# Optimization experiments

Measured on AMD Instinct MI355X. Metric: run time of the kernel, lower is better.

## Reference

```python
import jax, jax.numpy as jnp
import numpy as np
import math

N, M = 512, 31
INP, EMB, ATT = 64, 64, 64
NUM_RELS = 200
SELF_LOOP_IDX = NUM_RELS  # index num_rels is the self-loop relation


def setup_inputs() -> dict:
    key = jax.random.key(0)
    ks = jax.random.split(key, 11)
    s_w = 1.0 / math.sqrt(EMB)
    return {
        "h": jax.random.normal(ks[0], (N, INP), jnp.float32),
        "msg": jax.random.normal(ks[1], (N, M, EMB), jnp.float32),
        "msg_type": jax.random.randint(ks[2], (N, M), 0, NUM_RELS, jnp.int32),
        "r_label_node": jax.random.randint(ks[3], (N,), 0, NUM_RELS, jnp.int32),
        "r_label_msg": jax.random.randint(ks[4], (N, M), 0, NUM_RELS, jnp.int32),
        "W_self": jax.random.normal(ks[5], (INP, EMB), jnp.float32) * s_w,
        "Q": jax.random.normal(ks[6], (NUM_RELS + 1, EMB, ATT), jnp.float32) * s_w,
        "K": jax.random.normal(ks[7], (NUM_RELS + 1, EMB, ATT), jnp.float32) * s_w,
        "V": jax.random.normal(ks[8], (NUM_RELS + 1, EMB, ATT), jnp.float32) * s_w,
        "ffn_w": jax.random.normal(ks[9], (ATT, EMB), jnp.float32) * s_w,
        "ffn_b": jnp.zeros((EMB,), jnp.float32),
    }


def reference(h, msg, msg_type, r_label_node, r_label_msg, W_self, Q, K, V, ffn_w, ffn_b):
    curr = h @ W_self                                        # [N, EMB]
    x = jnp.concatenate([curr[:, None, :], msg], axis=1)     # [N, M+1, EMB]
    qv_idx = jnp.concatenate([r_label_node[:, None], r_label_msg], axis=1)  # [N, M+1]
    self_col = jnp.full((x.shape[0], 1), SELF_LOOP_IDX, msg_type.dtype)
    k_idx = jnp.concatenate([self_col, msg_type], axis=1)    # [N, M+1]
    # relation-indexed per-token projection weights (irregular gather)
    q = jnp.einsum("nme,nmea->nma", x, Q[qv_idx])            # [N, M+1, ATT]
    k = jnp.einsum("nme,nmea->nma", x, K[k_idx])             # [N, M+1, ATT]
    v = jnp.einsum("nme,nmea->nma", x, V[qv_idx])            # [N, M+1, ATT]
    scores = jnp.einsum("nqa,nka->nqk", q, k) / math.sqrt(ATT)
    # NOTE: original code applies softmax over dim=1 (the query axis)
    att = jax.nn.softmax(scores, axis=1)                     # [N, M+1, M+1]
    pooled = jnp.einsum("nqk,nka->nqa", att, v)[:, 0]        # [N, ATT]
    return pooled @ ffn_w + ffn_b                            # [N, EMB]
```

## Files before the change

kernel.cpp:

```cpp
#include <hip/hip_runtime.h>
#include <math.h>

#define NN 512
#define MM 31
#define TT 32
#define EE 64
#define NREL 200
#define NMAT 201
#define SELF_LOOP 200
#define QCAP 192
#define NT 6
#define WSTR 72
#define CPAD 32

typedef short  short8 __attribute__((ext_vector_type(8)));
typedef float  f32x4  __attribute__((ext_vector_type(4)));

__device__ __forceinline__ unsigned short f2bf(float f) {
    union { float f; unsigned int u; } a; a.f = f;
    unsigned int r = a.u + 0x7FFFu + ((a.u >> 16) & 1u);
    return (unsigned short)(r >> 16);
}
__device__ __forceinline__ float bf2f(unsigned short u) {
    union { unsigned int u; float f; } a; a.u = ((unsigned int)u) << 16;
    return a.f;
}

__global__ __launch_bounds__(256) void prep_convert_kernel(
    const float* __restrict__ h, const float* __restrict__ W_self,
    const float* __restrict__ Q, const float* __restrict__ K,
    const float* __restrict__ V,
    const int* __restrict__ msg_type, const int* __restrict__ r_label_node,
    const int* __restrict__ r_label_msg, const float* __restrict__ msg,
    int* __restrict__ cnt_q, int* __restrict__ cnt_k,
    int* __restrict__ list_q, int* __restrict__ list_k,
    unsigned short* __restrict__ wt_q, unsigned short* __restrict__ wt_k,
    unsigned short* __restrict__ wt_v,
    unsigned short* __restrict__ msg_bf, unsigned short* __restrict__ curr_bf,
    unsigned short* __restrict__ k_bf)
{
    const int bid = blockIdx.x, tid = threadIdx.x;

    if (bid < 3 * NMAT) {
        const int r   = bid % NMAT;
        const int mat = bid / NMAT;
        const float* src = (mat == 0 ? Q : mat == 1 ? K : V) + (size_t)r * EE * EE;
        unsigned short* dst = (mat == 0 ? wt_q : mat == 1 ? wt_k : wt_v)
                              + (size_t)r * EE * EE;
        __shared__ unsigned short t_s[EE * WSTR];
        {
            const int e = tid >> 2, aseg = (tid & 3) * 16;
            const float4* s4 = (const float4*)(src + e * EE + aseg);
            float4 f0 = s4[0], f1 = s4[1], f2 = s4[2], f3 = s4[3];
            unsigned short b[16] = {
                f2bf(f0.x), f2bf(f0.y), f2bf(f0.z), f2bf(f0.w),
                f2bf(f1.x), f2bf(f1.y), f2bf(f1.z), f2bf(f1.w),
                f2bf(f2.x), f2bf(f2.y), f2bf(f2.z), f2bf(f2.w),
                f2bf(f3.x), f2bf(f3.y), f2bf(f3.z), f2bf(f3.w) };
            unsigned short* d = &t_s[e * WSTR + aseg];
            *(short8*)d = *(short8*)&b[0];
            *(short8*)(d + 8) = *(short8*)&b[8];
        }
        __syncthreads();
        {
            const int a = tid >> 2, eseg = (tid & 3) * 16;
            unsigned short o[16];
#pragma unroll
            for (int j = 0; j < 16; ++j)
                o[j] = t_s[(eseg + j) * WSTR + a];
            unsigned short* d = dst + a * EE + eseg;
            *(short8*)d = *(short8*)&o[0];
            *(short8*)(d + 8) = *(short8*)&o[8];
        }
        return;
    }

    const int n = bid - 3 * NMAT;

    if (tid < MM) {
        int j  = n * MM + tid;
        int rl = r_label_msg[j];
        int p  = atomicAdd(&cnt_q[rl * CPAD], 1);
        if (p < QCAP) list_q[rl * QCAP + p] = n * TT + tid + 1;
        int mt = msg_type[j];
        int p2 = atomicAdd(&cnt_k[mt * CPAD], 1);
        if (p2 < QCAP) list_k[mt * QCAP + p2] = n * TT + tid + 1;
    } else if (tid == 63) {
        int r = r_label_node[n];
        int p = atomicAdd(&cnt_q[r * CPAD], 1);
        if (p < QCAP) list_q[r * QCAP + p] = n * TT;
    }

    if (tid < MM * EE / 8) {
        const float4* s4 = (const float4*)(msg + (size_t)n * MM * EE) + tid * 2;
        float4 f0 = s4[0], f1 = s4[1];
        unsigned short b[8] = { f2bf(f0.x), f2bf(f0.y), f2bf(f0.z), f2bf(f0.w),
                                f2bf(f1.x), f2bf(f1.y), f2bf(f1.z), f2bf(f1.w) };
        *(short8*)(msg_bf + (size_t)n * MM * EE + tid * 8) = *(short8*)b;
    }

    __shared__ float c_s[EE];
    if (tid < EE) {
        const float* hrow = h + n * EE;
        float acc = 0.f;
#pragma unroll 8
        for (int e = 0; e < EE; ++e)
            acc = fmaf(hrow[e], W_self[e * EE + tid], acc);
        curr_bf[n * EE + tid] = f2bf(acc);
        c_s[tid] = acc;
    }
    __syncthreads();
    if (tid < EE) {
        const float* K200 = K + (size_t)SELF_LOOP * EE * EE;
        float k0 = 0.f;
#pragma unroll 8
        for (int e = 0; e < EE; ++e)
            k0 = fmaf(c_s[e], K200[e * EE + tid], k0);
        k_bf[(size_t)n * TT * EE + tid] = f2bf(k0);
    }
}

__global__ __launch_bounds__(256) void proj_tile_kernel(
    const unsigned short* __restrict__ curr_bf,
    const unsigned short* __restrict__ msg_bf,
    const unsigned short* __restrict__ wt_q,
    const unsigned short* __restrict__ wt_k,
    const unsigned short* __restrict__ wt_v,
    const int* __restrict__ cnt_q, const int* __restrict__ cnt_k,
    const int* __restrict__ list_q, const int* __restrict__ list_k,
    unsigned short* __restrict__ q_bf, unsigned short* __restrict__ k_bf,
    unsigned short* __restrict__ v_bf)
{
    const int r    = blockIdx.x / NT;
    const int tile = blockIdx.x % NT;
    const int tid  = threadIdx.x;
    const int lane = tid & 63;
    const int wave = tid >> 6;
    const int col  = lane & 15;
    const int quad = lane >> 4;

    const int nq = min(cnt_q[r * CPAD], QCAP);
    const int nk = min(cnt_k[r * CPAD], QCAP);
    const int q0 = tile * 32;
    const bool do_q = q0 < nq;
    const bool do_k = q0 < nk;
    if (!do_q && !do_k) return;

    __shared__ unsigned short wq_s[EE * WSTR];
    __shared__ unsigned short wk_s[EE * WSTR];
    __shared__ unsigned short wv_s[EE * WSTR];
    __shared__ unsigned short x_s[64 * WSTR];
    __shared__ int tq_s[32], tk_s[32];

    {
        const int a = tid >> 2, seg = (tid & 3) * 16;
        const size_t go = (size_t)r * EE * EE + a * EE + seg;
        const int lo = a * WSTR + seg;
        if (do_q) {
            short8 w0 = *(const short8*)(wt_q + go);
            short8 w1 = *(const short8*)(wt_q + go + 8);
            *(short8*)&wq_s[lo] = w0; *(short8*)&wq_s[lo + 8] = w1;
            short8 v0 = *(const short8*)(wt_v + go);
            short8 v1 = *(const short8*)(wt_v + go + 8);
            *(short8*)&wv_s[lo] = v0; *(short8*)&wv_s[lo + 8] = v1;
        }
        if (do_k) {
            short8 k0_ = *(const short8*)(wt_k + go);
            short8 k1_ = *(const short8*)(wt_k + go + 8);
            *(short8*)&wk_s[lo] = k0_; *(short8*)&wk_s[lo + 8] = k1_;
        }
    }

    if (tid < 32) {
        tq_s[tid] = (do_q && q0 + tid < nq) ? list_q[r * QCAP + q0 + tid] : -1;
    } else if (tid < 64) {
        int i = tid - 32;
        tk_s[i] = (do_k && q0 + i < nk) ? list_k[r * QCAP + q0 + i] : -1;
    }

    {
        const int row = tid >> 2;
        const int seg = (tid & 3) * 16;
        const bool qside = row < 32;
        const int li = qside ? (q0 + row) : (q0 + row - 32);
        const bool valid = qside ? (do_q && li < nq) : (do_k && li < nk);
        if (valid) {
            int token = qside ? list_q[r * QCAP + li] : list_k[r * QCAP + li];
            int n = token >> 5, t = token & 31;
            const unsigned short* src = (t == 0)
                ? (curr_bf + n * EE)
                : (msg_bf + ((size_t)n * MM + (t - 1)) * EE);
            short8 s0 = *(const short8*)(src + seg);
            short8 s1 = *(const short8*)(src + seg + 8);
            unsigned short* d = &x_s[row * WSTR + seg];
            *(short8*)d = s0; *(short8*)(d + 8) = s1;
        }
    }
    __syncthreads();

    if (do_q) {
        const int mtile = wave & 1;
        const unsigned short* w_s = (wave >> 1) ? wv_s : wq_s;
        unsigned short* outp = (wave >> 1) ? v_bf : q_bf;
        const int m = mtile * 16 + col;
        f32x4 acc[4] = {{0,0,0,0},{0,0,0,0},{0,0,0,0},{0,0,0,0}};
#pragma unroll
        for (int kk = 0; kk < 2; ++kk) {
            short8 af = *(const short8*)&x_s[m * WSTR + kk * 32 + quad * 8];
#pragma unroll
            for (int nt = 0; nt < 4; ++nt) {
                short8 bf = *(const short8*)&w_s[(nt * 16 + col) * WSTR + kk * 32 + quad * 8];
                acc[nt] = __builtin_amdgcn_mfma_f32_16x16x32_bf16(af, bf, acc[nt], 0, 0, 0);
            }
        }
#pragma unroll
        for (int nt = 0; nt < 4; ++nt)
#pragma unroll
            for (int reg = 0; reg < 4; ++reg) {
                int rrow = mtile * 16 + quad * 4 + reg;
                int token = tq_s[rrow];
                if (token >= 0)
                    outp[(size_t)token * EE + nt * 16 + col] = f2bf(acc[nt][reg]);
            }
    }

    if (do_k) {
        const int mtile = wave & 1;
        const int nh = wave >> 1;
        const int m = 32 + mtile * 16 + col;
        f32x4 acc[2] = {{0,0,0,0},{0,0,0,0}};
#pragma unroll
        for (int kk = 0; kk < 2; ++kk) {
            short8 af = *(const short8*)&x_s[m * WSTR + kk * 32 + quad * 8];
#pragma unroll
            for (int j = 0; j < 2; ++j) {
                int nt = nh * 2 + j;
                short8 bf = *(const short8*)&wk_s[(nt * 16 + col) * WSTR + kk * 32 + quad * 8];
                acc[j] = __builtin_amdgcn_mfma_f32_16x16x32_bf16(af, bf, acc[j], 0, 0, 0);
            }
        }
#pragma unroll
        for (int j = 0; j < 2; ++j)
#pragma unroll
            for (int reg = 0; reg < 4; ++reg) {
                int rrow = mtile * 16 + quad * 4 + reg;
                int token = tk_s[rrow];
                if (token >= 0)
                    k_bf[(size_t)token * EE + (nh * 2 + j) * 16 + col] = f2bf(acc[j][reg]);
            }
    }
}

__global__ __launch_bounds__(256) void attn_kernel(
    const unsigned short* __restrict__ q_bf,
    const unsigned short* __restrict__ k_bf,
    const unsigned short* __restrict__ v_bf,
    const float* __restrict__ ffn_w, const float* __restrict__ ffn_b,
    float* __restrict__ out)
{
    const int n = blockIdx.x, tid = threadIdx.x;
    __shared__ float q_s[TT][68], k_s[TT][68], v_s[TT][68];
    __shared__ float s_s[TT][TT + 1];
    __shared__ float att0[TT];
    __shared__ float pooled[EE];

    {
        const int row = tid >> 3, c8 = (tid & 7) * 8;
        const size_t go = (size_t)n * TT * EE + row * EE + c8;
        short8 q8 = *(const short8*)(q_bf + go);
        short8 k8 = *(const short8*)(k_bf + go);
        short8 v8 = *(const short8*)(v_bf + go);
#pragma unroll
        for (int j = 0; j < 8; ++j) {
            q_s[row][c8 + j] = bf2f(((unsigned short*)&q8)[j]);
            k_s[row][c8 + j] = bf2f(((unsigned short*)&k8)[j]);
            v_s[row][c8 + j] = bf2f(((unsigned short*)&v8)[j]);
        }
    }
    __syncthreads();

    {
        const int ki = tid & 31;
        for (int qi = tid >> 5; qi < TT; qi += 8) {
            const float4* qp = (const float4*)&q_s[qi][0];
            const float4* kp = (const float4*)&k_s[ki][0];
            float acc = 0.f;
            for (int e4 = 0; e4 < EE / 4; ++e4) {
                float4 a = qp[e4], b = kp[e4];
                acc += a.x * b.x + a.y * b.y + a.z * b.z + a.w * b.w;
            }
            s_s[qi][ki] = acc * 0.125f;
        }
    }
    __syncthreads();

    if (tid < TT) {
        float mx = -INFINITY;
        for (int qi = 0; qi < TT; ++qi) mx = fmaxf(mx, s_s[qi][tid]);
        float sum = 0.f;
        for (int qi = 0; qi < TT; ++qi) sum += __expf(s_s[qi][tid] - mx);
        att0[tid] = __expf(s_s[0][tid] - mx) / sum;
    }
    __syncthreads();

    if (tid < EE) {
        float acc = 0.f;
        for (int ki = 0; ki < TT; ++ki)
            acc = fmaf(att0[ki], v_s[ki][tid], acc);
        pooled[tid] = acc;
    }
    __syncthreads();

    if (tid < EE) {
        float acc = ffn_b[tid];
        for (int a = 0; a < EE; ++a)
            acc = fmaf(pooled[a], ffn_w[a * EE + tid], acc);
        out[n * EE + tid] = acc;
    }
}

extern "C" void kernel_launch(void* const* d_in, const int* in_sizes, int n_in,
                              void* d_out, int out_size, void* d_ws, size_t ws_size,
                              hipStream_t stream) {
    const float* h            = (const float*)d_in[0];
    const float* msg          = (const float*)d_in[1];
    const int*   msg_type     = (const int*)  d_in[2];
    const int*   r_label_node = (const int*)  d_in[3];
    const int*   r_label_msg  = (const int*)  d_in[4];
    const float* W_self       = (const float*)d_in[5];
    const float* Q            = (const float*)d_in[6];
    const float* K            = (const float*)d_in[7];
    const float* V            = (const float*)d_in[8];
    const float* ffn_w        = (const float*)d_in[9];
    const float* ffn_b        = (const float*)d_in[10];
    float*       out          = (float*)d_out;

    int* cnt_q  = (int*)d_ws;
    int* cnt_k  = cnt_q + NREL * CPAD;
    int* list_q = cnt_k + NREL * CPAD;
    int* list_k = list_q + NREL * QCAP;
    unsigned short* wt_q = (unsigned short*)(list_k + NREL * QCAP);
    unsigned short* wt_k = wt_q + (size_t)NMAT * EE * EE;
    unsigned short* wt_v = wt_k + (size_t)NMAT * EE * EE;
    unsigned short* msg_bf  = wt_v + (size_t)NMAT * EE * EE;
    unsigned short* curr_bf = msg_bf + (size_t)NN * MM * EE;
    unsigned short* q_bf = curr_bf + NN * EE;
    unsigned short* k_bf = q_bf + (size_t)NN * TT * EE;
    unsigned short* v_bf = k_bf + (size_t)NN * TT * EE;

    hipMemsetAsync(cnt_q, 0, 2 * NREL * CPAD * sizeof(int), stream);
    prep_convert_kernel<<<3 * NMAT + NN, 256, 0, stream>>>(
        h, W_self, Q, K, V, msg_type, r_label_node, r_label_msg, msg,
        cnt_q, cnt_k, list_q, list_k, wt_q, wt_k, wt_v,
        msg_bf, curr_bf, k_bf);
    proj_tile_kernel<<<NREL * NT, 256, 0, stream>>>(
        curr_bf, msg_bf, wt_q, wt_k, wt_v, cnt_q, cnt_k, list_q, list_k,
        q_bf, k_bf, v_bf);
    attn_kernel<<<NN, 256, 0, stream>>>(q_bf, k_bf, v_bf, ffn_w, ffn_b, out);
}
```

Baseline: 107.3 us.

## Drop LDS staging in projection and use MFMA for attention scores

The projection kernel no longer stages weights, token rows and token lists in shared memory. Each wave loads MFMA fragments straight from global memory, and the __syncthreads barrier goes away. The attention kernel now computes the 32x32 score matrix with bf16 MFMA directly from global q/k, reads v from global in the pooling step, and unrolls its small loops. The goal is to cut LDS traffic, conversion work and barriers, at the cost of redundant uncoalesced global fragment loads that rely on cache hits.

```diff
diff --git a/kernel.cpp b/kernel.cpp
--- a/kernel.cpp
+++ b/kernel.cpp
@@ -146,108 +146,73 @@
     const bool do_k = q0 < nk;
     if (!do_q && !do_k) return;
 
-    __shared__ unsigned short wq_s[EE * WSTR];
-    __shared__ unsigned short wk_s[EE * WSTR];
-    __shared__ unsigned short wv_s[EE * WSTR];
-    __shared__ unsigned short x_s[64 * WSTR];
-    __shared__ int tq_s[32], tk_s[32];
-
-    {
-        const int a = tid >> 2, seg = (tid & 3) * 16;
-        const size_t go = (size_t)r * EE * EE + a * EE + seg;
-        const int lo = a * WSTR + seg;
-        if (do_q) {
-            short8 w0 = *(const short8*)(wt_q + go);
-            short8 w1 = *(const short8*)(wt_q + go + 8);
-            *(short8*)&wq_s[lo] = w0; *(short8*)&wq_s[lo + 8] = w1;
-            short8 v0 = *(const short8*)(wt_v + go);
-            short8 v1 = *(const short8*)(wt_v + go + 8);
-            *(short8*)&wv_s[lo] = v0; *(short8*)&wv_s[lo + 8] = v1;
-        }
-        if (do_k) {
-            short8 k0_ = *(const short8*)(wt_k + go);
-            short8 k1_ = *(const short8*)(wt_k + go + 8);
-            *(short8*)&wk_s[lo] = k0_; *(short8*)&wk_s[lo + 8] = k1_;
-        }
-    }
-
-    if (tid < 32) {
-        tq_s[tid] = (do_q && q0 + tid < nq) ? list_q[r * QCAP + q0 + tid] : -1;
-    } else if (tid < 64) {
-        int i = tid - 32;
-        tk_s[i] = (do_k && q0 + i < nk) ? list_k[r * QCAP + q0 + i] : -1;
-    }
-
-    {
-        const int row = tid >> 2;
-        const int seg = (tid & 3) * 16;
-        const bool qside = row < 32;
-        const int li = qside ? (q0 + row) : (q0 + row - 32);
-        const bool valid = qside ? (do_q && li < nq) : (do_k && li < nk);
-        if (valid) {
-            int token = qside ? list_q[r * QCAP + li] : list_k[r * QCAP + li];
-            int n = token >> 5, t = token & 31;
-            const unsigned short* src = (t == 0)
-                ? (curr_bf + n * EE)
-                : (msg_bf + ((size_t)n * MM + (t - 1)) * EE);
-            short8 s0 = *(const short8*)(src + seg);
-            short8 s1 = *(const short8*)(src + seg + 8);
-            unsigned short* d = &x_s[row * WSTR + seg];
-            *(short8*)d = s0; *(short8*)(d + 8) = s1;
-        }
-    }
-    __syncthreads();
+    const size_t wbase = (size_t)r * EE * EE;
 
     if (do_q) {
         const int mtile = wave & 1;
-        const unsigned short* w_s = (wave >> 1) ? wv_s : wq_s;
+        const unsigned short* wmat = ((wave >> 1) ? wt_v : wt_q) + wbase;
         unsigned short* outp = (wave >> 1) ? v_bf : q_bf;
-        const int m = mtile * 16 + col;
-        f32x4 acc[4] = {{0,0,0,0},{0,0,0,0},{0,0,0,0},{0,0,0,0}};
-#pragma unroll
-        for (int kk = 0; kk < 2; ++kk) {
-            short8 af = *(const short8*)&x_s[m * WSTR + kk * 32 + quad * 8];
-#pragma unroll
-            for (int nt = 0; nt < 4; ++nt) {
-                short8 bf = *(const short8*)&w_s[(nt * 16 + col) * WSTR + kk * 32 + quad * 8];
-                acc[nt] = __builtin_amdgcn_mfma_f32_16x16x32_bf16(af, bf, acc[nt], 0, 0, 0);
+        const int arow = q0 + mtile * 16 + col;
+        int atok = (arow < nq) ? list_q[r * QCAP + arow] : 0;
+        {
+            int an = atok >> 5, at = atok & 31;
+            const unsigned short* aptr = at
+                ? (msg_bf + ((size_t)an * MM + (at - 1)) * EE)
+                : (curr_bf + (size_t)an * EE);
+            f32x4 acc[4] = {{0,0,0,0},{0,0,0,0},{0,0,0,0},{0,0,0,0}};
+#pragma unroll
+            for (int kk = 0; kk < 2; ++kk) {
+                short8 af = *(const short8*)(aptr + kk * 32 + quad * 8);
+#pragma unroll
+                for (int nt = 0; nt < 4; ++nt) {
+                    short8 bf = *(const short8*)(wmat + (nt * 16 + col) * EE + kk * 32 + quad * 8);
+                    acc[nt] = __builtin_amdgcn_mfma_f32_16x16x32_bf16(af, bf, acc[nt], 0, 0, 0);
+                }
             }
-        }
-#pragma unroll
-        for (int nt = 0; nt < 4; ++nt)
 #pragma unroll
             for (int reg = 0; reg < 4; ++reg) {
-                int rrow = mtile * 16 + quad * 4 + reg;
-                int token = tq_s[rrow];
-                if (token >= 0)
-                    outp[(size_t)token * EE + nt * 16 + col] = f2bf(acc[nt][reg]);
+                int rrow = q0 + mtile * 16 + quad * 4 + reg;
+                if (rrow < nq) {
+                    int token = list_q[r * QCAP + rrow];
+#pragma unroll
+                    for (int nt = 0; nt < 4; ++nt)
+                        outp[(size_t)token * EE + nt * 16 + col] = f2bf(acc[nt][reg]);
+                }
             }
+        }
     }
 
     if (do_k) {
         const int mtile = wave & 1;
         const int nh = wave >> 1;
-        const int m = 32 + mtile * 16 + col;
+        const int arow = q0 + mtile * 16 + col;
+        int atok = (arow < nk) ? list_k[r * QCAP + arow] : 0;
+        int an = atok >> 5, at = atok & 31;
+        const unsigned short* aptr = at
+            ? (msg_bf + ((size_t)an * MM + (at - 1)) * EE)
+            : (curr_bf + (size_t)an * EE);
+        const unsigned short* wmat = wt_k + wbase;
         f32x4 acc[2] = {{0,0,0,0},{0,0,0,0}};
 #pragma unroll
         for (int kk = 0; kk < 2; ++kk) {
-            short8 af = *(const short8*)&x_s[m * WSTR + kk * 32 + quad * 8];
+            short8 af = *(const short8*)(aptr + kk * 32 + quad * 8);
 #pragma unroll
             for (int j = 0; j < 2; ++j) {
                 int nt = nh * 2 + j;
-                short8 bf = *(const short8*)&wk_s[(nt * 16 + col) * WSTR + kk * 32 + quad * 8];
+                short8 bf = *(const short8*)(wmat + (nt * 16 + col) * EE + kk * 32 + quad * 8);
                 acc[j] = __builtin_amdgcn_mfma_f32_16x16x32_bf16(af, bf, acc[j], 0, 0, 0);
             }
         }
 #pragma unroll
-        for (int j = 0; j < 2; ++j)
-#pragma unroll
-            for (int reg = 0; reg < 4; ++reg) {
-                int rrow = mtile * 16 + quad * 4 + reg;
-                int token = tk_s[rrow];
-                if (token >= 0)
+        for (int reg = 0; reg < 4; ++reg) {
+            int rrow = q0 + mtile * 16 + quad * 4 + reg;
+            if (rrow < nk) {
+                int token = list_k[r * QCAP + rrow];
+#pragma unroll
+                for (int j = 0; j < 2; ++j)
                     k_bf[(size_t)token * EE + (nh * 2 + j) * 16 + col] = f2bf(acc[j][reg]);
             }
+        }
     }
 }
 
@@ -259,60 +224,53 @@
     float* __restrict__ out)
 {
     const int n = blockIdx.x, tid = threadIdx.x;
-    __shared__ float q_s[TT][68], k_s[TT][68], v_s[TT][68];
+    const int lane = tid & 63, wave = tid >> 6;
+    const int col = lane & 15, quad = lane >> 4;
     __shared__ float s_s[TT][TT + 1];
     __shared__ float att0[TT];
     __shared__ float pooled[EE];
 
     {
-        const int row = tid >> 3, c8 = (tid & 7) * 8;
-        const size_t go = (size_t)n * TT * EE + row * EE + c8;
-        short8 q8 = *(const short8*)(q_bf + go);
-        short8 k8 = *(const short8*)(k_bf + go);
-        short8 v8 = *(const short8*)(v_bf + go);
-#pragma unroll
-        for (int j = 0; j < 8; ++j) {
-            q_s[row][c8 + j] = bf2f(((unsigned short*)&q8)[j]);
-            k_s[row][c8 + j] = bf2f(((unsigned short*)&k8)[j]);
-            v_s[row][c8 + j] = bf2f(((unsigned short*)&v8)[j]);
-        }
-    }
-    __syncthreads();
-
-    {
-        const int ki = tid & 31;
-        for (int qi = tid >> 5; qi < TT; qi += 8) {
-            const float4* qp = (const float4*)&q_s[qi][0];
-            const float4* kp = (const float4*)&k_s[ki][0];
-            float acc = 0.f;
-            for (int e4 = 0; e4 < EE / 4; ++e4) {
-                float4 a = qp[e4], b = kp[e4];
-                acc += a.x * b.x + a.y * b.y + a.z * b.z + a.w * b.w;
-            }
-            s_s[qi][ki] = acc * 0.125f;
-        }
+        const int mi = wave & 1, ni = wave >> 1;
+        const unsigned short* qrow = q_bf + ((size_t)n * TT + mi * 16 + col) * EE;
+        const unsigned short* krow = k_bf + ((size_t)n * TT + ni * 16 + col) * EE;
+        f32x4 acc = {0, 0, 0, 0};
+#pragma unroll
+        for (int kk = 0; kk < 2; ++kk) {
+            short8 a = *(const short8*)(qrow + kk * 32 + quad * 8);
+            short8 b = *(const short8*)(krow + kk * 32 + quad * 8);
+            acc = __builtin_amdgcn_mfma_f32_16x16x32_bf16(a, b, acc, 0, 0, 0);
+        }
+#pragma unroll
+        for (int reg = 0; reg < 4; ++reg)
+            s_s[mi * 16 + quad * 4 + reg][ni * 16 + col] = acc[reg] * 0.125f;
     }
     __syncthreads();
 
     if (tid < TT) {
         float mx = -INFINITY;
+#pragma unroll
         for (int qi = 0; qi < TT; ++qi) mx = fmaxf(mx, s_s[qi][tid]);
         float sum = 0.f;
+#pragma unroll
         for (int qi = 0; qi < TT; ++qi) sum += __expf(s_s[qi][tid] - mx);
         att0[tid] = __expf(s_s[0][tid] - mx) / sum;
     }
     __syncthreads();
 
     if (tid < EE) {
+        const unsigned short* vp = v_bf + (size_t)n * TT * EE + tid;
         float acc = 0.f;
+#pragma unroll 8
         for (int ki = 0; ki < TT; ++ki)
-            acc = fmaf(att0[ki], v_s[ki][tid], acc);
+            acc = fmaf(att0[ki], bf2f(vp[ki * EE]), acc);
         pooled[tid] = acc;
     }
     __syncthreads();
 
     if (tid < EE) {
         float acc = ffn_b[tid];
+#pragma unroll 8
         for (int a = 0; a < EE; ++a)
             acc = fmaf(pooled[a], ffn_w[a * EE + tid], acc);
         out[n * EE + tid] = acc;
```

Result: slower. 111.3 us (+3.7%).
